# Kernel optimization log

Hardware: AMD Instinct MI355X
Metric: run time of the kernel (lower is better)

## Reference

```python
import jax, jax.numpy as jnp
import numpy as np

HID = 512
HEADS = 8
D = HID // HEADS          # att_size = 64
B = 64                    # number of graphs
L = 1024                  # bonds per graph (equal-length scopes)
SCALE = D ** (-0.5)
EPS = 1e-5


def setup_inputs() -> dict:
    key = jax.random.key(0)
    ks = jax.random.split(key, 9)
    f = lambda k, s, sc=1.0: jax.random.normal(k, s, dtype=jnp.float32) * sc
    edge_attr = f(ks[0], (B * L, HID))
    # contiguous equal-length scopes: (start, length) per graph
    scopes = np.stack([np.arange(B, dtype=np.int64) * L,
                       np.full(B, L, dtype=np.int64)], axis=1)
    return {
        "edge_attr": edge_attr,
        "batch_scopes": jnp.asarray(scopes),
        "Wq": f(ks[1], (HID, HID), 0.03),   # torch Linear weight [out, in]
        "Wk": f(ks[2], (HID, HID), 0.03),
        "Wv": f(ks[3], (HID, HID), 0.03),
        "Wr": f(ks[4], (D, D), 0.1),
        "w_alpha": f(ks[5], (D,)),
        "w_beta": f(ks[6], (D,)),
        "Wo": f(ks[7], (HID, HID), 0.03),
        "bo": jnp.zeros((HID,), jnp.float32),
        "ln_g": jnp.ones((HID,), jnp.float32),
        "ln_b": jnp.zeros((HID,), jnp.float32),
    }


def reference(edge_attr, batch_scopes, Wq, Wk, Wv, Wr, w_alpha, w_beta,
              Wo, bo, ln_g, ln_b):
    # Scopes are contiguous, equal length L -> pad_sequence == reshape
    padded = edge_attr.reshape(B, L, HID)

    def proj(W):  # (B, L, HID) @ W.T -> (B, heads, L, D)
        return jnp.einsum('blh,dh->bld', padded, W).reshape(B, L, HEADS, D).transpose(0, 2, 1, 3)

    b_q = proj(Wq)
    b_k = proj(Wk)
    b_v = proj(Wv)

    # softmax over the head-feature dim (faithful to dim=-1 in torch code)
    alpha = jax.nn.softmax(b_q * w_alpha * SCALE, axis=-1)
    global_q = jnp.sum(alpha * b_q, axis=2)            # (B, heads, D), sum over L

    p = global_q[:, :, None, :] * b_k                  # (B, heads, L, D)
    beta = jax.nn.softmax(p * w_beta * SCALE, axis=-1)
    global_k = jnp.sum(beta * p, axis=2)               # (B, heads, D)

    kv = global_k[:, :, None, :] * b_v                 # (B, heads, L, D)
    kv_out = jnp.einsum('bhld,ed->bhle', kv, Wr)
    att = jax.nn.relu(kv_out + b_q)                    # dropout p=0 (eval)

    att = att.transpose(0, 2, 1, 3).reshape(B, L, HID)
    out = jnp.einsum('blh,oh->blo', att, Wo) + bo

    # LayerNorm over last dim
    mu = jnp.mean(out, axis=-1, keepdims=True)
    var = jnp.mean((out - mu) ** 2, axis=-1, keepdims=True)
    out = (out - mu) * jax.lax.rsqrt(var + EPS) * ln_g + ln_b

    # unpad + concat == flatten for equal-length contiguous scopes
    return out.reshape(B * L, HID)
```

## Files before the change

### kernel.cpp

```cpp
#include <hip/hip_runtime.h>
#include <stdint.h>


#define SCALE_F 0.125f
#define EPSF 1e-5f

typedef __attribute__((ext_vector_type(8))) short short8;
typedef __attribute__((ext_vector_type(4))) float float4v;
typedef unsigned short ushort_t;

__device__ __forceinline__ ushort_t f2bf(float f) {
  uint32_t u = __builtin_bit_cast(uint32_t, f);
  u += 0x7fffu + ((u >> 16) & 1u);
  return (ushort_t)(u >> 16);
}
__device__ __forceinline__ float bf2f(ushort_t s) {
  uint32_t u = ((uint32_t)s) << 16;
  return __builtin_bit_cast(float, u);
}

__device__ __forceinline__ void gload16(const void* g, void* l) {
  __builtin_amdgcn_global_load_lds(
      (__attribute__((address_space(1))) char*)(char*)const_cast<void*>(g),
      (__attribute__((address_space(3))) char*)(char*)l, 16, 0, 0);
}

#define SBAR() __builtin_amdgcn_s_barrier()
#define LGKM0() do { __builtin_amdgcn_sched_barrier(0);                 \
                     asm volatile("s_waitcnt lgkmcnt(0)" ::: "memory"); \
                     __builtin_amdgcn_sched_barrier(0); } while (0)

__global__ __launch_bounds__(256) void cvt_all(const float* __restrict__ X,
                                               const float* __restrict__ Wq,
                                               const float* __restrict__ Wk,
                                               const float* __restrict__ Wv,
                                               const float* __restrict__ Wo,
                                               ushort_t* __restrict__ Xb,
                                               ushort_t* __restrict__ Wqkv,
                                               ushort_t* __restrict__ Wob) {
  const int i = blockIdx.x * 256 + threadIdx.x;
  if (i < 4194304) {
    const float4v* src = (const float4v*)X;
    float4v v0 = src[(size_t)i * 2];
    float4v v1 = src[(size_t)i * 2 + 1];
    short8 o;
#pragma unroll
    for (int j = 0; j < 4; ++j) {
      o[j]     = (short)f2bf(v0[j]);
      o[j + 4] = (short)f2bf(v1[j]);
    }
    ((short8*)Xb)[i] = o;
  } else {
    const int j = i - 4194304;
    if (j < 262144)        Wqkv[j] = f2bf(Wq[j]);
    else if (j < 524288)   Wqkv[j] = f2bf(Wk[j - 262144]);
    else if (j < 786432)   Wqkv[j] = f2bf(Wv[j - 524288]);
    else                   Wob[j - 786432] = f2bf(Wo[j - 786432]);
  }
}

__global__ __launch_bounds__(512, 2) void gemm8p(const ushort_t* __restrict__ A,
                                                 const ushort_t* __restrict__ Bm,
                                                 ushort_t* __restrict__ C) {
  __shared__ __align__(16) char ldsA[65536];
  __shared__ __align__(16) char ldsB[65536];
  const int swz = (blockIdx.x & 7) * 192 + (blockIdx.x >> 3);
  const int tm = swz / 6, tn = swz % 6;
  const int row0 = tm * 256, col0 = tn * 256;
  const int tid = threadIdx.x, wid = tid >> 6, lane = tid & 63;
  const int wr = wid >> 2, wc = wid & 3;
  const int lr = lane & 15, lk = lane >> 4;
  const int xr = (lr & 7) << 4;

  auto stageA = [&](int t) {
    const int kt = t;
#pragma unroll
    for (int i = 0; i < 4; ++i) {
      const int o = i * 8192 + wid * 1024 + lane * 16;
      const int r = o >> 7, x = o & 127;
      gload16((const char*)A + (size_t)(row0 + r) * 1024 + kt * 128 + (x ^ ((r & 7) << 4)),
              ldsA + (t & 1) * 32768 + i * 8192 + wid * 1024);
    }
  };
  auto stageB = [&](int t) {
    const int kt = t;
#pragma unroll
    for (int i = 0; i < 4; ++i) {
      const int o = i * 8192 + wid * 1024 + lane * 16;
      const int r = o >> 7, x = o & 127;
      gload16((const char*)Bm + (size_t)(col0 + r) * 1024 + kt * 128 + (x ^ ((r & 7) << 4)),
              ldsB + (t & 1) * 32768 + i * 8192 + wid * 1024);
    }
  };
  auto rdA = [&](int sl, int mi, int kk) -> short8 {
    return *(const short8*)(ldsA + sl * 32768 + (wr * 128 + mi * 16 + lr) * 128 +
                            ((kk * 64 + lk * 16) ^ xr));
  };
  auto rdB = [&](int sl, int ni, int kk) -> short8 {
    return *(const short8*)(ldsB + sl * 32768 + (wc * 64 + ni * 16 + lr) * 128 +
                            ((kk * 64 + lk * 16) ^ xr));
  };

  float4v acc[8][4] = {};

  stageA(0); stageB(0);
  stageA(1); stageB(1);
  asm volatile("s_waitcnt vmcnt(8)" ::: "memory");
  SBAR();

#pragma unroll
  for (int t = 0; t < 8; ++t) {
    const int sl = t & 1;
    short8 a0[4][2], a1[4][2], b[4][2];
#pragma unroll
    for (int mi = 0; mi < 4; ++mi)
#pragma unroll
      for (int kk = 0; kk < 2; ++kk) a0[mi][kk] = rdA(sl, mi, kk);
#pragma unroll
    for (int ni = 0; ni < 4; ++ni)
#pragma unroll
      for (int kk = 0; kk < 2; ++kk) b[ni][kk] = rdB(sl, ni, kk);
    LGKM0();
    SBAR();
    if (t + 2 < 8) stageB(t + 2);
#pragma unroll
    for (int mi = 0; mi < 4; ++mi)
#pragma unroll
      for (int kk = 0; kk < 2; ++kk) a1[mi][kk] = rdA(sl, mi + 4, kk);
    __builtin_amdgcn_s_setprio(1);
#pragma unroll
    for (int kk = 0; kk < 2; ++kk)
#pragma unroll
      for (int mi = 0; mi < 4; ++mi)
#pragma unroll
        for (int ni = 0; ni < 4; ++ni)
          acc[mi][ni] = __builtin_amdgcn_mfma_f32_16x16x32_bf16(a0[mi][kk], b[ni][kk], acc[mi][ni], 0, 0, 0);
    __builtin_amdgcn_s_setprio(0);
    LGKM0();
    SBAR();
    if (t + 2 < 8) stageA(t + 2);
    __builtin_amdgcn_s_setprio(1);
#pragma unroll
    for (int kk = 0; kk < 2; ++kk)
#pragma unroll
      for (int mi = 0; mi < 4; ++mi)
#pragma unroll
        for (int ni = 0; ni < 4; ++ni)
          acc[mi + 4][ni] = __builtin_amdgcn_mfma_f32_16x16x32_bf16(a1[mi][kk], b[ni][kk], acc[mi + 4][ni], 0, 0, 0);
    __builtin_amdgcn_s_setprio(0);
    __builtin_amdgcn_sched_barrier(0);
    if (t < 6) {
      asm volatile("s_waitcnt vmcnt(8)" ::: "memory");
    } else if (t == 6) {
      asm volatile("s_waitcnt vmcnt(0)" ::: "memory");
    }
    SBAR();
  }

#pragma unroll
  for (int mi = 0; mi < 8; ++mi)
#pragma unroll
    for (int ni = 0; ni < 4; ++ni) {
      const int col = col0 + wc * 64 + ni * 16 + lr;
#pragma unroll
      for (int r = 0; r < 4; ++r) {
        const int row = row0 + wr * 128 + mi * 16 + lk * 4 + r;
        C[(size_t)row * 1536 + col] = f2bf(acc[mi][ni][r]);
      }
    }
}

__global__ __launch_bounds__(256) void reduce_gq(const ushort_t* __restrict__ QKV,
                                                 const float* __restrict__ w_alpha,
                                                 float* __restrict__ gq_part) {
  const int bx = blockIdx.x, bh = bx >> 2, ch = bx & 3;
  const int b = bh >> 3, h = bh & 7;
  const int tid = threadIdx.x, wid = tid >> 6, lane = tid & 63;
  const int rsub = lane >> 3, dch = lane & 7;
  __shared__ float red[4][64];
  float wa[8];
#pragma unroll
  for (int j = 0; j < 8; ++j) wa[j] = w_alpha[dch * 8 + j] * SCALE_F;
  const size_t base = (size_t)b * 1024 + ch * 256;
  float acc[8] = {0, 0, 0, 0, 0, 0, 0, 0};
  for (int it = 0; it < 8; ++it) {
    const size_t t = base + it * 32 + wid * 8 + rsub;
    short8 raw = *(const short8*)(QKV + t * 1536 + h * 64 + dch * 8);
    float q[8], s[8];
#pragma unroll
    for (int j = 0; j < 8; ++j) { q[j] = bf2f((ushort_t)raw[j]); s[j] = q[j] * wa[j]; }
    float m = s[0];
#pragma unroll
    for (int j = 1; j < 8; ++j) m = fmaxf(m, s[j]);
    m = fmaxf(m, __shfl_xor(m, 1)); m = fmaxf(m, __shfl_xor(m, 2)); m = fmaxf(m, __shfl_xor(m, 4));
    float e[8], sum = 0.f;
#pragma unroll
    for (int j = 0; j < 8; ++j) { e[j] = __expf(s[j] - m); sum += e[j]; }
    sum += __shfl_xor(sum, 1); sum += __shfl_xor(sum, 2); sum += __shfl_xor(sum, 4);
    const float inv = 1.0f / sum;
#pragma unroll
    for (int j = 0; j < 8; ++j) acc[j] += e[j] * inv * q[j];
  }
#pragma unroll
  for (int msk = 8; msk < 64; msk <<= 1)
#pragma unroll
    for (int j = 0; j < 8; ++j) acc[j] += __shfl_xor(acc[j], msk);
  if (lane < 8) {
#pragma unroll
    for (int j = 0; j < 8; ++j) red[wid][lane * 8 + j] = acc[j];
  }
  __syncthreads();
  if (tid < 64)
    gq_part[(size_t)bx * 64 + tid] = red[0][tid] + red[1][tid] + red[2][tid] + red[3][tid];
}

__global__ __launch_bounds__(256) void reduce_gk(const ushort_t* __restrict__ QKV,
                                                 const float* __restrict__ w_beta,
                                                 const float* __restrict__ gq_part,
                                                 float* __restrict__ gk_part) {
  const int bx = blockIdx.x, bh = bx >> 2, ch = bx & 3;
  const int b = bh >> 3, h = bh & 7;
  const int tid = threadIdx.x, wid = tid >> 6, lane = tid & 63;
  const int rsub = lane >> 3, dch = lane & 7;
  __shared__ float red[4][64];
  __shared__ float gq_s[64];
  if (tid < 64) {
    float s = 0.f;
#pragma unroll
    for (int c = 0; c < 4; ++c) s += gq_part[(size_t)(bh * 4 + c) * 64 + tid];
    gq_s[tid] = s;
  }
  __syncthreads();
  float wb[8], gq[8];
#pragma unroll
  for (int j = 0; j < 8; ++j) {
    wb[j] = w_beta[dch * 8 + j] * SCALE_F;
    gq[j] = gq_s[dch * 8 + j];
  }
  const size_t base = (size_t)b * 1024 + ch * 256;
  float acc[8] = {0, 0, 0, 0, 0, 0, 0, 0};
  for (int it = 0; it < 8; ++it) {
    const size_t t = base + it * 32 + wid * 8 + rsub;
    short8 raw = *(const short8*)(QKV + t * 1536 + 512 + h * 64 + dch * 8);
    float p[8], s[8];
#pragma unroll
    for (int j = 0; j < 8; ++j) { p[j] = gq[j] * bf2f((ushort_t)raw[j]); s[j] = p[j] * wb[j]; }
    float m = s[0];
#pragma unroll
    for (int j = 1; j < 8; ++j) m = fmaxf(m, s[j]);
    m = fmaxf(m, __shfl_xor(m, 1)); m = fmaxf(m, __shfl_xor(m, 2)); m = fmaxf(m, __shfl_xor(m, 4));
    float e[8], sum = 0.f;
#pragma unroll
    for (int j = 0; j < 8; ++j) { e[j] = __expf(s[j] - m); sum += e[j]; }
    sum += __shfl_xor(sum, 1); sum += __shfl_xor(sum, 2); sum += __shfl_xor(sum, 4);
    const float inv = 1.0f / sum;
#pragma unroll
    for (int j = 0; j < 8; ++j) acc[j] += e[j] * inv * p[j];
  }
#pragma unroll
  for (int msk = 8; msk < 64; msk <<= 1)
#pragma unroll
    for (int j = 0; j < 8; ++j) acc[j] += __shfl_xor(acc[j], msk);
  if (lane < 8) {
#pragma unroll
    for (int j = 0; j < 8; ++j) red[wid][lane * 8 + j] = acc[j];
  }
  __syncthreads();
  if (tid < 64)
    gk_part[(size_t)bx * 64 + tid] = red[0][tid] + red[1][tid] + red[2][tid] + red[3][tid];
}

__global__ __launch_bounds__(512, 2) void att_out(const ushort_t* __restrict__ QKV,
                                                  const float* __restrict__ Wr,
                                                  const float* __restrict__ gk_part,
                                                  const ushort_t* __restrict__ Wob,
                                                  const float* __restrict__ bo,
                                                  const float* __restrict__ lng,
                                                  const float* __restrict__ lnb,
                                                  float* __restrict__ out) {
  __shared__ __align__(16) ushort_t att_s[128 * 520];
  __shared__ float gk_s[8][64];
  __shared__ float red_s[4][128][2];
  __shared__ float tot_s[128][2];
  const int bx = blockIdx.x;
  const int t0 = bx * 128;
  const int bg = bx >> 3;
  const int tid = threadIdx.x, wid = tid >> 6, lane = tid & 63;
  const int lr = lane & 15, lk = lane >> 4;

  {
    const int h = tid >> 6, d = tid & 63;
    const int bh = bg * 8 + h;
    float s = 0.f;
#pragma unroll
    for (int c = 0; c < 4; ++c) s += gk_part[(size_t)(bh * 4 + c) * 64 + d];
    gk_s[h][d] = s;
  }
  __syncthreads();

  short8 bfi[4][2];
#pragma unroll
  for (int ni = 0; ni < 4; ++ni)
#pragma unroll
    for (int ks = 0; ks < 2; ++ks)
#pragma unroll
      for (int j = 0; j < 8; ++j)
        bfi[ni][ks][j] = (ni * 16 + lr == ks * 32 + lk * 8 + j) ? (short)0x3F80 : (short)0;

  const size_t trow = (size_t)t0 + wid * 16 + lr;
  for (int h = 0; h < 8; ++h) {
    short8 bfr[4][2];
#pragma unroll
    for (int ni = 0; ni < 4; ++ni)
#pragma unroll
      for (int ks = 0; ks < 2; ++ks) {
        const int e = ni * 16 + lr;
        const int k0 = ks * 32 + lk * 8;
        const float4v w0 = *(const float4v*)(Wr + e * 64 + k0);
        const float4v w1 = *(const float4v*)(Wr + e * 64 + k0 + 4);
        const float4v g0 = *(const float4v*)(&gk_s[h][k0]);
        const float4v g1 = *(const float4v*)(&gk_s[h][k0 + 4]);
        short8 rfrag;
#pragma unroll
        for (int j = 0; j < 4; ++j) {
          rfrag[j]     = (short)f2bf(w0[j] * g0[j]);
          rfrag[j + 4] = (short)f2bf(w1[j] * g1[j]);
        }
        bfr[ni][ks] = rfrag;
      }
    float4v pacc[4] = {};
#pragma unroll
    for (int ks = 0; ks < 2; ++ks) {
      const short8 av  = *(const short8*)(QKV + trow * 1536 + 1024 + h * 64 + ks * 32 + lk * 8);
      const short8 aqv = *(const short8*)(QKV + trow * 1536 +        h * 64 + ks * 32 + lk * 8);
#pragma unroll
      for (int ni = 0; ni < 4; ++ni) {
        pacc[ni] = __builtin_amdgcn_mfma_f32_16x16x32_bf16(av,  bfr[ni][ks], pacc[ni], 0, 0, 0);
        pacc[ni] = __builtin_amdgcn_mfma_f32_16x16x32_bf16(aqv, bfi[ni][ks], pacc[ni], 0, 0, 0);
      }
    }
#pragma unroll
    for (int ni = 0; ni < 4; ++ni)
#pragma unroll
      for (int r = 0; r < 4; ++r)
        att_s[(wid * 16 + lk * 4 + r) * 520 + h * 64 + ni * 16 + lr] =
            f2bf(fmaxf(pacc[ni][r], 0.0f));
  }
  __syncthreads();

  const int wr = wid >> 2, wc = wid & 3;
  float4v acc[4][8] = {};
#pragma unroll 4
  for (int kc = 0; kc < 16; ++kc) {
    short8 a[4], bf[8];
#pragma unroll
    for (int mi = 0; mi < 4; ++mi)
      a[mi] = *(const short8*)(att_s + (wr * 64 + mi * 16 + lr) * 520 + kc * 32 + lk * 8);
#pragma unroll
    for (int ni = 0; ni < 8; ++ni)
      bf[ni] = *(const short8*)(Wob + (size_t)(wc * 128 + ni * 16 + lr) * 512 + kc * 32 + lk * 8);
#pragma unroll
    for (int mi = 0; mi < 4; ++mi)
#pragma unroll
      for (int ni = 0; ni < 8; ++ni)
        acc[mi][ni] = __builtin_amdgcn_mfma_f32_16x16x32_bf16(a[mi], bf[ni], acc[mi][ni], 0, 0, 0);
  }

  float bov[8], gv[8], bv[8];
#pragma unroll
  for (int ni = 0; ni < 8; ++ni) {
    const int c = wc * 128 + ni * 16 + lr;
    bov[ni] = bo[c]; gv[ni] = lng[c]; bv[ni] = lnb[c];
  }
#pragma unroll
  for (int mi = 0; mi < 4; ++mi)
#pragma unroll
    for (int ni = 0; ni < 8; ++ni)
#pragma unroll
      for (int r = 0; r < 4; ++r)
        acc[mi][ni][r] += bov[ni];
#pragma unroll
  for (int mi = 0; mi < 4; ++mi)
#pragma unroll
    for (int r = 0; r < 4; ++r) {
      float s = 0.f, q = 0.f;
#pragma unroll
      for (int ni = 0; ni < 8; ++ni) { const float v = acc[mi][ni][r]; s += v; q += v * v; }
      s += __shfl_xor(s, 1); q += __shfl_xor(q, 1);
      s += __shfl_xor(s, 2); q += __shfl_xor(q, 2);
      s += __shfl_xor(s, 4); q += __shfl_xor(q, 4);
      s += __shfl_xor(s, 8); q += __shfl_xor(q, 8);
      if (lr == 0) {
        const int rb = wr * 64 + mi * 16 + lk * 4 + r;
        red_s[wc][rb][0] = s;
        red_s[wc][rb][1] = q;
      }
    }
  __syncthreads();
  if (tid < 128) {
    tot_s[tid][0] = red_s[0][tid][0] + red_s[1][tid][0] + red_s[2][tid][0] + red_s[3][tid][0];
    tot_s[tid][1] = red_s[0][tid][1] + red_s[1][tid][1] + red_s[2][tid][1] + red_s[3][tid][1];
  }
  __syncthreads();
#pragma unroll
  for (int mi = 0; mi < 4; ++mi)
#pragma unroll
    for (int r = 0; r < 4; ++r) {
      const int rb = wr * 64 + mi * 16 + lk * 4 + r;
      const float mu = tot_s[rb][0] * (1.f / 512.f);
      const float var = tot_s[rb][1] * (1.f / 512.f) - mu * mu;
      const float rs = rsqrtf(var + EPSF);
      float* op = out + (size_t)(t0 + rb) * 512 + wc * 128 + lr;
#pragma unroll
      for (int ni = 0; ni < 8; ++ni)
        op[ni * 16] = (acc[mi][ni][r] - mu) * rs * gv[ni] + bv[ni];
    }
}

extern "C" void kernel_launch(void* const* d_in, const int* in_sizes, int n_in,
                              void* d_out, int out_size, void* d_ws, size_t ws_size,
                              hipStream_t stream) {
  const float* X       = (const float*)d_in[0];
  const float* Wq      = (const float*)d_in[2];
  const float* Wk      = (const float*)d_in[3];
  const float* Wv      = (const float*)d_in[4];
  const float* Wr      = (const float*)d_in[5];
  const float* w_alpha = (const float*)d_in[6];
  const float* w_beta  = (const float*)d_in[7];
  const float* Wo      = (const float*)d_in[8];
  const float* bo      = (const float*)d_in[9];
  const float* ln_g    = (const float*)d_in[10];
  const float* ln_b    = (const float*)d_in[11];

  char* ws = (char*)d_ws;
  ushort_t* Xb      = (ushort_t*)(ws);
  ushort_t* Wqkv    = (ushort_t*)(ws + 67108864);
  ushort_t* Wob     = (ushort_t*)(ws + 68681728);
  ushort_t* QKV     = (ushort_t*)(ws + 69206016);
  float*    gq_part = (float*)(ws + 270532608);
  float*    gk_part = (float*)(ws + 271056896);
  float* out = (float*)d_out;

  hipLaunchKernelGGL(cvt_all, dim3(20480), dim3(256), 0, stream,
                     X, Wq, Wk, Wv, Wo, Xb, Wqkv, Wob);
  hipLaunchKernelGGL(gemm8p, dim3(1536), dim3(512), 0, stream, Xb, Wqkv, QKV);
  hipLaunchKernelGGL(reduce_gq, dim3(2048), dim3(256), 0, stream, QKV, w_alpha, gq_part);
  hipLaunchKernelGGL(reduce_gk, dim3(2048), dim3(256), 0, stream,
                     QKV, w_beta, gq_part, gk_part);
  hipLaunchKernelGGL(att_out, dim3(512), dim3(512), 0, stream,
                     QKV, Wr, gk_part, Wob, bo, ln_g, ln_b, out);
}
```

Before: 325.2 us.

## Precompute per-head Wr*gk matrices and retile att_out with swizzled LDS and prefetch

Adds a small mgen kernel that builds the bf16 Wr·diag(global_k) matrix once per graph-head, so att_out no longer recomputes and converts it in every block. att_out moves to 64-row tiles with 256 threads and 1024 blocks. It loads all V/Q fragments up front, stores attention output into LDS with an XOR swizzle instead of padding, and double-buffers Wo fragment loads in the output GEMM. This trades one extra launch and reuse of the Xb workspace region for less redundant work, fewer bank conflicts and better latency hiding, at the cost of higher register pressure.

```diff
diff --git a/kernel.cpp b/kernel.cpp
--- a/kernel.cpp
+++ b/kernel.cpp
@@ -270,34 +270,47 @@
     gk_part[(size_t)bx * 64 + tid] = red[0][tid] + red[1][tid] + red[2][tid] + red[3][tid];
 }
 
-__global__ __launch_bounds__(512, 2) void att_out(const ushort_t* __restrict__ QKV,
-                                                  const float* __restrict__ Wr,
-                                                  const float* __restrict__ gk_part,
+__global__ __launch_bounds__(256) void mgen(const float* __restrict__ Wr,
+                                            const float* __restrict__ gk_part,
+                                            ushort_t* __restrict__ Mall) {
+  const int bh = blockIdx.x, tid = threadIdx.x;
+  __shared__ float gk_s[64];
+  if (tid < 64) {
+    float s = 0.f;
+#pragma unroll
+    for (int c = 0; c < 4; ++c) s += gk_part[(size_t)(bh * 4 + c) * 64 + tid];
+    gk_s[tid] = s;
+  }
+  __syncthreads();
+  const int e = tid >> 2, k0 = (tid & 3) * 16;
+  ushort_t* dst = Mall + (size_t)bh * 4096 + e * 64 + k0;
+  const float* wsrc = Wr + e * 64 + k0;
+#pragma unroll
+  for (int half = 0; half < 2; ++half) {
+    short8 o;
+#pragma unroll
+    for (int j = 0; j < 8; ++j)
+      o[j] = (short)f2bf(wsrc[half * 8 + j] * gk_s[k0 + half * 8 + j]);
+    *(short8*)(dst + half * 8) = o;
+  }
+}
+
+__global__ __launch_bounds__(256, 2) void att_out(const ushort_t* __restrict__ QKV,
+                                                  const ushort_t* __restrict__ Mall,
                                                   const ushort_t* __restrict__ Wob,
                                                   const float* __restrict__ bo,
                                                   const float* __restrict__ lng,
                                                   const float* __restrict__ lnb,
                                                   float* __restrict__ out) {
-  __shared__ __align__(16) ushort_t att_s[128 * 520];
-  __shared__ float gk_s[8][64];
-  __shared__ float red_s[4][128][2];
-  __shared__ float tot_s[128][2];
+  __shared__ __align__(16) char att_s[65536];
+  __shared__ float red_s[4][64][2];
+  __shared__ float tot_s[64][2];
   const int bx = blockIdx.x;
-  const int t0 = bx * 128;
-  const int bg = bx >> 3;
+  const int t0 = bx * 64;
+  const int bg = bx >> 4;
   const int tid = threadIdx.x, wid = tid >> 6, lane = tid & 63;
   const int lr = lane & 15, lk = lane >> 4;
 
-  {
-    const int h = tid >> 6, d = tid & 63;
-    const int bh = bg * 8 + h;
-    float s = 0.f;
-#pragma unroll
-    for (int c = 0; c < 4; ++c) s += gk_part[(size_t)(bh * 4 + c) * 64 + d];
-    gk_s[h][d] = s;
-  }
-  __syncthreads();
-
   short8 bfi[4][2];
 #pragma unroll
   for (int ni = 0; ni < 4; ++ni)
@@ -308,62 +321,75 @@
         bfi[ni][ks][j] = (ni * 16 + lr == ks * 32 + lk * 8 + j) ? (short)0x3F80 : (short)0;
 
   const size_t trow = (size_t)t0 + wid * 16 + lr;
+  short8 vv[16], qq[16];
+#pragma unroll
+  for (int h = 0; h < 8; ++h)
+#pragma unroll
+    for (int ks = 0; ks < 2; ++ks) {
+      vv[h * 2 + ks] = *(const short8*)(QKV + trow * 1536 + 1024 + h * 64 + ks * 32 + lk * 8);
+      qq[h * 2 + ks] = *(const short8*)(QKV + trow * 1536 +        h * 64 + ks * 32 + lk * 8);
+    }
+#pragma unroll
   for (int h = 0; h < 8; ++h) {
+    const ushort_t* Mh = Mall + ((size_t)bg * 8 + h) * 4096;
     short8 bfr[4][2];
 #pragma unroll
     for (int ni = 0; ni < 4; ++ni)
 #pragma unroll
-      for (int ks = 0; ks < 2; ++ks) {
-        const int e = ni * 16 + lr;
-        const int k0 = ks * 32 + lk * 8;
-        const float4v w0 = *(const float4v*)(Wr + e * 64 + k0);
-        const float4v w1 = *(const float4v*)(Wr + e * 64 + k0 + 4);
-        const float4v g0 = *(const float4v*)(&gk_s[h][k0]);
-        const float4v g1 = *(const float4v*)(&gk_s[h][k0 + 4]);
-        short8 rfrag;
-#pragma unroll
-        for (int j = 0; j < 4; ++j) {
-          rfrag[j]     = (short)f2bf(w0[j] * g0[j]);
-          rfrag[j + 4] = (short)f2bf(w1[j] * g1[j]);
-        }
-        bfr[ni][ks] = rfrag;
+      for (int ks = 0; ks < 2; ++ks)
+        bfr[ni][ks] = *(const short8*)(Mh + (ni * 16 + lr) * 64 + ks * 32 + lk * 8);
+    float4v pacc[4] = {};
+#pragma unroll
+    for (int ks = 0; ks < 2; ++ks)
+#pragma unroll
+      for (int ni = 0; ni < 4; ++ni) {
+        pacc[ni] = __builtin_amdgcn_mfma_f32_16x16x32_bf16(vv[h * 2 + ks], bfr[ni][ks], pacc[ni], 0, 0, 0);
+        pacc[ni] = __builtin_amdgcn_mfma_f32_16x16x32_bf16(qq[h * 2 + ks], bfi[ni][ks], pacc[ni], 0, 0, 0);
       }
-    float4v pacc[4] = {};
-#pragma unroll
-    for (int ks = 0; ks < 2; ++ks) {
-      const short8 av  = *(const short8*)(QKV + trow * 1536 + 1024 + h * 64 + ks * 32 + lk * 8);
-      const short8 aqv = *(const short8*)(QKV + trow * 1536 +        h * 64 + ks * 32 + lk * 8);
-#pragma unroll
-      for (int ni = 0; ni < 4; ++ni) {
-        pacc[ni] = __builtin_amdgcn_mfma_f32_16x16x32_bf16(av,  bfr[ni][ks], pacc[ni], 0, 0, 0);
-        pacc[ni] = __builtin_amdgcn_mfma_f32_16x16x32_bf16(aqv, bfi[ni][ks], pacc[ni], 0, 0, 0);
+#pragma unroll
+    for (int ni = 0; ni < 4; ++ni)
+#pragma unroll
+      for (int r = 0; r < 4; ++r) {
+        const int row = wid * 16 + lk * 4 + r;
+        const int colb = h * 128 + ni * 32 + lr * 2;
+        *(ushort_t*)(att_s + row * 1024 + (colb ^ ((row & 7) << 4))) =
+            f2bf(fmaxf(pacc[ni][r], 0.0f));
       }
-    }
-#pragma unroll
-    for (int ni = 0; ni < 4; ++ni)
-#pragma unroll
-      for (int r = 0; r < 4; ++r)
-        att_s[(wid * 16 + lk * 4 + r) * 520 + h * 64 + ni * 16 + lr] =
-            f2bf(fmaxf(pacc[ni][r], 0.0f));
-  }
-  __syncthreads();
-
-  const int wr = wid >> 2, wc = wid & 3;
+  }
+  __syncthreads();
+
+  const int wc = wid;
+  auto ldBf = [&](short8* d, int kc) {
+#pragma unroll
+    for (int ni = 0; ni < 8; ++ni)
+      d[ni] = *(const short8*)(Wob + (size_t)(wc * 128 + ni * 16 + lr) * 512 + kc * 32 + lk * 8);
+  };
+  auto rdAtt = [&](short8* a, int kc) {
+#pragma unroll
+    for (int mi = 0; mi < 4; ++mi) {
+      const int row = mi * 16 + lr;
+      a[mi] = *(const short8*)(att_s + row * 1024 + ((kc * 64 + lk * 16) ^ ((row & 7) << 4)));
+    }
+  };
   float4v acc[4][8] = {};
-#pragma unroll 4
-  for (int kc = 0; kc < 16; ++kc) {
-    short8 a[4], bf[8];
+  short8 bA[8], bB[8], aT[4];
+  ldBf(bA, 0);
+#pragma unroll
+  for (int k2 = 0; k2 < 8; ++k2) {
+    ldBf(bB, 2 * k2 + 1);
+    rdAtt(aT, 2 * k2);
 #pragma unroll
     for (int mi = 0; mi < 4; ++mi)
-      a[mi] = *(const short8*)(att_s + (wr * 64 + mi * 16 + lr) * 520 + kc * 32 + lk * 8);
-#pragma unroll
-    for (int ni = 0; ni < 8; ++ni)
-      bf[ni] = *(const short8*)(Wob + (size_t)(wc * 128 + ni * 16 + lr) * 512 + kc * 32 + lk * 8);
+#pragma unroll
+      for (int ni = 0; ni < 8; ++ni)
+        acc[mi][ni] = __builtin_amdgcn_mfma_f32_16x16x32_bf16(aT[mi], bA[ni], acc[mi][ni], 0, 0, 0);
+    if (k2 < 7) ldBf(bA, 2 * k2 + 2);
+    rdAtt(aT, 2 * k2 + 1);
 #pragma unroll
     for (int mi = 0; mi < 4; ++mi)
 #pragma unroll
       for (int ni = 0; ni < 8; ++ni)
-        acc[mi][ni] = __builtin_amdgcn_mfma_f32_16x16x32_bf16(a[mi], bf[ni], acc[mi][ni], 0, 0, 0);
+        acc[mi][ni] = __builtin_amdgcn_mfma_f32_16x16x32_bf16(aT[mi], bB[ni], acc[mi][ni], 0, 0, 0);
   }
 
   float bov[8], gv[8], bv[8];
@@ -391,13 +417,13 @@
       s += __shfl_xor(s, 4); q += __shfl_xor(q, 4);
       s += __shfl_xor(s, 8); q += __shfl_xor(q, 8);
       if (lr == 0) {
-        const int rb = wr * 64 + mi * 16 + lk * 4 + r;
+        const int rb = mi * 16 + lk * 4 + r;
         red_s[wc][rb][0] = s;
         red_s[wc][rb][1] = q;
       }
     }
   __syncthreads();
-  if (tid < 128) {
+  if (tid < 64) {
     tot_s[tid][0] = red_s[0][tid][0] + red_s[1][tid][0] + red_s[2][tid][0] + red_s[3][tid][0];
     tot_s[tid][1] = red_s[0][tid][1] + red_s[1][tid][1] + red_s[2][tid][1] + red_s[3][tid][1];
   }
@@ -406,7 +432,7 @@
   for (int mi = 0; mi < 4; ++mi)
 #pragma unroll
     for (int r = 0; r < 4; ++r) {
-      const int rb = wr * 64 + mi * 16 + lk * 4 + r;
+      const int rb = mi * 16 + lk * 4 + r;
       const float mu = tot_s[rb][0] * (1.f / 512.f);
       const float var = tot_s[rb][1] * (1.f / 512.f) - mu * mu;
       const float rs = rsqrtf(var + EPSF);
@@ -434,6 +460,7 @@
 
   char* ws = (char*)d_ws;
   ushort_t* Xb      = (ushort_t*)(ws);
+  ushort_t* Mall    = (ushort_t*)(ws);
   ushort_t* Wqkv    = (ushort_t*)(ws + 67108864);
   ushort_t* Wob     = (ushort_t*)(ws + 68681728);
   ushort_t* QKV     = (ushort_t*)(ws + 69206016);
@@ -447,6 +474,7 @@
   hipLaunchKernelGGL(reduce_gq, dim3(2048), dim3(256), 0, stream, QKV, w_alpha, gq_part);
   hipLaunchKernelGGL(reduce_gk, dim3(2048), dim3(256), 0, stream,
                      QKV, w_beta, gq_part, gk_part);
-  hipLaunchKernelGGL(att_out, dim3(512), dim3(512), 0, stream,
-                     QKV, Wr, gk_part, Wob, bo, ln_g, ln_b, out);
-}
+  hipLaunchKernelGGL(mgen, dim3(512), dim3(256), 0, stream, Wr, gk_part, Mall);
+  hipLaunchKernelGGL(att_out, dim3(1024), dim3(256), 0, stream,
+                     QKV, Mall, Wob, bo, ln_g, ln_b, out);
+}
```

New measurement: 341.1 us. 4.9% more time.

## Halve GEMM K-tile to 32KB LDS and precompute scaled Wr matrices per head

Applied to the files above, without the earlier changes.

The QKV GEMM now stages 64-byte K slices instead of 128-byte ones. That halves LDS use to 64KB per block and doubles the loop trip count, with an adjusted XOR swizzle and vmcnt waits. This is likely meant to improve occupancy or let two blocks fit per CU. A new mgen kernel builds the per-(graph, head) bf16 matrices Wr*gk once and stores them in the workspace, aliased over the no-longer-needed Xb buffer. att_out then loads them directly instead of recomputing them in every block. The change adds one kernel launch and extra global traffic in exchange for less redundant work, and the GEMM pays more barriers per K step.

```diff
diff --git a/kernel.cpp b/kernel.cpp
--- a/kernel.cpp
+++ b/kernel.cpp
@@ -59,99 +59,87 @@
   }
 }
 
-__global__ __launch_bounds__(512, 2) void gemm8p(const ushort_t* __restrict__ A,
+__global__ __launch_bounds__(512, 2) void gemm32(const ushort_t* __restrict__ A,
                                                  const ushort_t* __restrict__ Bm,
                                                  ushort_t* __restrict__ C) {
-  __shared__ __align__(16) char ldsA[65536];
-  __shared__ __align__(16) char ldsB[65536];
+  __shared__ __align__(16) char ldsA[32768];
+  __shared__ __align__(16) char ldsB[32768];
   const int swz = (blockIdx.x & 7) * 192 + (blockIdx.x >> 3);
   const int tm = swz / 6, tn = swz % 6;
   const int row0 = tm * 256, col0 = tn * 256;
   const int tid = threadIdx.x, wid = tid >> 6, lane = tid & 63;
   const int wr = wid >> 2, wc = wid & 3;
   const int lr = lane & 15, lk = lane >> 4;
-  const int xr = (lr & 7) << 4;
-
-  auto stageA = [&](int t) {
-    const int kt = t;
-#pragma unroll
-    for (int i = 0; i < 4; ++i) {
+  const int xr = ((lr >> 1) & 3) << 4;
+
+  auto stageA = [&](int s) {
+#pragma unroll
+    for (int i = 0; i < 2; ++i) {
       const int o = i * 8192 + wid * 1024 + lane * 16;
-      const int r = o >> 7, x = o & 127;
-      gload16((const char*)A + (size_t)(row0 + r) * 1024 + kt * 128 + (x ^ ((r & 7) << 4)),
-              ldsA + (t & 1) * 32768 + i * 8192 + wid * 1024);
+      const int r = o >> 6, x = o & 63;
+      gload16((const char*)A + (size_t)(row0 + r) * 1024 + s * 64 + (x ^ ((((r) >> 1) & 3) << 4)),
+              ldsA + (s & 1) * 16384 + i * 8192 + wid * 1024);
     }
   };
-  auto stageB = [&](int t) {
-    const int kt = t;
-#pragma unroll
-    for (int i = 0; i < 4; ++i) {
+  auto stageB = [&](int s) {
+#pragma unroll
+    for (int i = 0; i < 2; ++i) {
       const int o = i * 8192 + wid * 1024 + lane * 16;
-      const int r = o >> 7, x = o & 127;
-      gload16((const char*)Bm + (size_t)(col0 + r) * 1024 + kt * 128 + (x ^ ((r & 7) << 4)),
-              ldsB + (t & 1) * 32768 + i * 8192 + wid * 1024);
+      const int r = o >> 6, x = o & 63;
+      gload16((const char*)Bm + (size_t)(col0 + r) * 1024 + s * 64 + (x ^ ((((r) >> 1) & 3) << 4)),
+              ldsB + (s & 1) * 16384 + i * 8192 + wid * 1024);
     }
   };
-  auto rdA = [&](int sl, int mi, int kk) -> short8 {
-    return *(const short8*)(ldsA + sl * 32768 + (wr * 128 + mi * 16 + lr) * 128 +
-                            ((kk * 64 + lk * 16) ^ xr));
+  auto rdA = [&](int sl, int mi) -> short8 {
+    const int row = wr * 128 + mi * 16 + lr;
+    return *(const short8*)(ldsA + sl * 16384 + row * 64 + ((lk * 16) ^ xr));
   };
-  auto rdB = [&](int sl, int ni, int kk) -> short8 {
-    return *(const short8*)(ldsB + sl * 32768 + (wc * 64 + ni * 16 + lr) * 128 +
-                            ((kk * 64 + lk * 16) ^ xr));
+  auto rdB = [&](int sl, int ni) -> short8 {
+    const int row = wc * 64 + ni * 16 + lr;
+    return *(const short8*)(ldsB + sl * 16384 + row * 64 + ((lk * 16) ^ xr));
   };
 
   float4v acc[8][4] = {};
 
   stageA(0); stageB(0);
   stageA(1); stageB(1);
-  asm volatile("s_waitcnt vmcnt(8)" ::: "memory");
+  asm volatile("s_waitcnt vmcnt(4)" ::: "memory");
   SBAR();
 
-#pragma unroll
-  for (int t = 0; t < 8; ++t) {
-    const int sl = t & 1;
-    short8 a0[4][2], a1[4][2], b[4][2];
-#pragma unroll
-    for (int mi = 0; mi < 4; ++mi)
-#pragma unroll
-      for (int kk = 0; kk < 2; ++kk) a0[mi][kk] = rdA(sl, mi, kk);
-#pragma unroll
-    for (int ni = 0; ni < 4; ++ni)
-#pragma unroll
-      for (int kk = 0; kk < 2; ++kk) b[ni][kk] = rdB(sl, ni, kk);
+#pragma unroll 2
+  for (int s = 0; s < 16; ++s) {
+    const int sl = s & 1;
+    short8 a0[4], a1[4], b[4];
+#pragma unroll
+    for (int mi = 0; mi < 4; ++mi) a0[mi] = rdA(sl, mi);
+#pragma unroll
+    for (int ni = 0; ni < 4; ++ni) b[ni] = rdB(sl, ni);
     LGKM0();
     SBAR();
-    if (t + 2 < 8) stageB(t + 2);
+    if (s + 2 < 16) stageB(s + 2);
+#pragma unroll
+    for (int mi = 0; mi < 4; ++mi) a1[mi] = rdA(sl, mi + 4);
+    __builtin_amdgcn_s_setprio(1);
 #pragma unroll
     for (int mi = 0; mi < 4; ++mi)
 #pragma unroll
-      for (int kk = 0; kk < 2; ++kk) a1[mi][kk] = rdA(sl, mi + 4, kk);
-    __builtin_amdgcn_s_setprio(1);
-#pragma unroll
-    for (int kk = 0; kk < 2; ++kk)
-#pragma unroll
-      for (int mi = 0; mi < 4; ++mi)
-#pragma unroll
-        for (int ni = 0; ni < 4; ++ni)
-          acc[mi][ni] = __builtin_amdgcn_mfma_f32_16x16x32_bf16(a0[mi][kk], b[ni][kk], acc[mi][ni], 0, 0, 0);
+      for (int ni = 0; ni < 4; ++ni)
+        acc[mi][ni] = __builtin_amdgcn_mfma_f32_16x16x32_bf16(a0[mi], b[ni], acc[mi][ni], 0, 0, 0);
     __builtin_amdgcn_s_setprio(0);
     LGKM0();
     SBAR();
-    if (t + 2 < 8) stageA(t + 2);
+    if (s + 2 < 16) stageA(s + 2);
     __builtin_amdgcn_s_setprio(1);
 #pragma unroll
-    for (int kk = 0; kk < 2; ++kk)
-#pragma unroll
-      for (int mi = 0; mi < 4; ++mi)
-#pragma unroll
-        for (int ni = 0; ni < 4; ++ni)
-          acc[mi + 4][ni] = __builtin_amdgcn_mfma_f32_16x16x32_bf16(a1[mi][kk], b[ni][kk], acc[mi + 4][ni], 0, 0, 0);
+    for (int mi = 0; mi < 4; ++mi)
+#pragma unroll
+      for (int ni = 0; ni < 4; ++ni)
+        acc[mi + 4][ni] = __builtin_amdgcn_mfma_f32_16x16x32_bf16(a1[mi], b[ni], acc[mi + 4][ni], 0, 0, 0);
     __builtin_amdgcn_s_setprio(0);
     __builtin_amdgcn_sched_barrier(0);
-    if (t < 6) {
-      asm volatile("s_waitcnt vmcnt(8)" ::: "memory");
-    } else if (t == 6) {
+    if (s < 14) {
+      asm volatile("s_waitcnt vmcnt(4)" ::: "memory");
+    } else if (s == 14) {
       asm volatile("s_waitcnt vmcnt(0)" ::: "memory");
     }
     SBAR();
@@ -270,16 +258,39 @@
     gk_part[(size_t)bx * 64 + tid] = red[0][tid] + red[1][tid] + red[2][tid] + red[3][tid];
 }
 
+__global__ __launch_bounds__(256) void mgen(const float* __restrict__ Wr,
+                                            const float* __restrict__ gk_part,
+                                            ushort_t* __restrict__ Mall) {
+  const int bh = blockIdx.x, tid = threadIdx.x;
+  __shared__ float gk_s[64];
+  if (tid < 64) {
+    float s = 0.f;
+#pragma unroll
+    for (int c = 0; c < 4; ++c) s += gk_part[(size_t)(bh * 4 + c) * 64 + tid];
+    gk_s[tid] = s;
+  }
+  __syncthreads();
+  const int e = tid >> 2, k0 = (tid & 3) * 16;
+  ushort_t* dst = Mall + (size_t)bh * 4096 + e * 64 + k0;
+  const float* wsrc = Wr + e * 64 + k0;
+#pragma unroll
+  for (int half = 0; half < 2; ++half) {
+    short8 o;
+#pragma unroll
+    for (int j = 0; j < 8; ++j)
+      o[j] = (short)f2bf(wsrc[half * 8 + j] * gk_s[k0 + half * 8 + j]);
+    *(short8*)(dst + half * 8) = o;
+  }
+}
+
 __global__ __launch_bounds__(512, 2) void att_out(const ushort_t* __restrict__ QKV,
-                                                  const float* __restrict__ Wr,
-                                                  const float* __restrict__ gk_part,
+                                                  const ushort_t* __restrict__ Mall,
                                                   const ushort_t* __restrict__ Wob,
                                                   const float* __restrict__ bo,
                                                   const float* __restrict__ lng,
                                                   const float* __restrict__ lnb,
                                                   float* __restrict__ out) {
   __shared__ __align__(16) ushort_t att_s[128 * 520];
-  __shared__ float gk_s[8][64];
   __shared__ float red_s[4][128][2];
   __shared__ float tot_s[128][2];
   const int bx = blockIdx.x;
@@ -288,16 +299,6 @@
   const int tid = threadIdx.x, wid = tid >> 6, lane = tid & 63;
   const int lr = lane & 15, lk = lane >> 4;
 
-  {
-    const int h = tid >> 6, d = tid & 63;
-    const int bh = bg * 8 + h;
-    float s = 0.f;
-#pragma unroll
-    for (int c = 0; c < 4; ++c) s += gk_part[(size_t)(bh * 4 + c) * 64 + d];
-    gk_s[h][d] = s;
-  }
-  __syncthreads();
-
   short8 bfi[4][2];
 #pragma unroll
   for (int ni = 0; ni < 4; ++ni)
@@ -309,25 +310,13 @@
 
   const size_t trow = (size_t)t0 + wid * 16 + lr;
   for (int h = 0; h < 8; ++h) {
+    const ushort_t* Mh = Mall + ((size_t)bg * 8 + h) * 4096;
     short8 bfr[4][2];
 #pragma unroll
     for (int ni = 0; ni < 4; ++ni)
 #pragma unroll
-      for (int ks = 0; ks < 2; ++ks) {
-        const int e = ni * 16 + lr;
-        const int k0 = ks * 32 + lk * 8;
-        const float4v w0 = *(const float4v*)(Wr + e * 64 + k0);
-        const float4v w1 = *(const float4v*)(Wr + e * 64 + k0 + 4);
-        const float4v g0 = *(const float4v*)(&gk_s[h][k0]);
-        const float4v g1 = *(const float4v*)(&gk_s[h][k0 + 4]);
-        short8 rfrag;
-#pragma unroll
-        for (int j = 0; j < 4; ++j) {
-          rfrag[j]     = (short)f2bf(w0[j] * g0[j]);
-          rfrag[j + 4] = (short)f2bf(w1[j] * g1[j]);
-        }
-        bfr[ni][ks] = rfrag;
-      }
+      for (int ks = 0; ks < 2; ++ks)
+        bfr[ni][ks] = *(const short8*)(Mh + (ni * 16 + lr) * 64 + ks * 32 + lk * 8);
     float4v pacc[4] = {};
 #pragma unroll
     for (int ks = 0; ks < 2; ++ks) {
@@ -434,6 +423,7 @@
 
   char* ws = (char*)d_ws;
   ushort_t* Xb      = (ushort_t*)(ws);
+  ushort_t* Mall    = (ushort_t*)(ws);
   ushort_t* Wqkv    = (ushort_t*)(ws + 67108864);
   ushort_t* Wob     = (ushort_t*)(ws + 68681728);
   ushort_t* QKV     = (ushort_t*)(ws + 69206016);
@@ -443,10 +433,11 @@
 
   hipLaunchKernelGGL(cvt_all, dim3(20480), dim3(256), 0, stream,
                      X, Wq, Wk, Wv, Wo, Xb, Wqkv, Wob);
-  hipLaunchKernelGGL(gemm8p, dim3(1536), dim3(512), 0, stream, Xb, Wqkv, QKV);
+  hipLaunchKernelGGL(gemm32, dim3(1536), dim3(512), 0, stream, Xb, Wqkv, QKV);
   hipLaunchKernelGGL(reduce_gq, dim3(2048), dim3(256), 0, stream, QKV, w_alpha, gq_part);
   hipLaunchKernelGGL(reduce_gk, dim3(2048), dim3(256), 0, stream,
                      QKV, w_beta, gq_part, gk_part);
+  hipLaunchKernelGGL(mgen, dim3(512), dim3(256), 0, stream, Wr, gk_part, Mall);
   hipLaunchKernelGGL(att_out, dim3(512), dim3(512), 0, stream,
-                     QKV, Wr, gk_part, Wob, bo, ln_g, ln_b, out);
-}
+                     QKV, Mall, Wob, bo, ln_g, ln_b, out);
+}
```

Measured after the change: 354.7 us. +9.1%, slower.
